# Optimization experiments

Hardware: AMD Instinct MI355X
Metric: run time of the kernel (lower is better)

The kernel has to match this reference:

```python
import jax, jax.numpy as jnp
import numpy as np

# ViT-Tiny + Performer attention (eval mode: dropout/droppath are no-ops)
B = 64
IMG, PATCH, GRID = 224, 16, 14
NPATCH, NTOK = 196, 197
EMBED, HEADS, HEAD_DIM = 192, 3, 64
DEPTH, FEAT, MLP, NCLS = 12, 256, 768, 1000
EXIT_IDXS = [4, 8, 12]
LN_EPS = 1e-5


def _ln(x, w, b):
    mu = x.mean(-1, keepdims=True)
    var = ((x - mu) ** 2).mean(-1, keepdims=True)
    return (x - mu) / jnp.sqrt(var + LN_EPS) * w + b


def setup_inputs() -> dict:
    key = jax.random.key(0)
    ks = jax.random.split(key, 16)
    n = lambda k, shape, s=0.02: jax.random.normal(k, shape, jnp.float32) * s
    inp = {}
    inp["x"] = jax.random.normal(ks[0], (B, 3, IMG, IMG), jnp.float32)
    inp["patch_w"] = n(ks[1], (EMBED, 3, PATCH, PATCH))
    inp["patch_b"] = jnp.zeros((EMBED,), jnp.float32)
    inp["pe_norm_w"] = jnp.ones((EMBED,), jnp.float32)
    inp["pe_norm_b"] = jnp.zeros((EMBED,), jnp.float32)
    inp["cls_token"] = n(ks[2], (1, 1, EMBED))
    inp["pos_embed"] = n(ks[3], (1, NTOK, EMBED))
    inp["norm1_w"] = jnp.ones((DEPTH, EMBED), jnp.float32)
    inp["norm1_b"] = jnp.zeros((DEPTH, EMBED), jnp.float32)
    inp["qkv_w"] = n(ks[4], (DEPTH, EMBED, 3 * EMBED))
    inp["qkv_b"] = jnp.zeros((DEPTH, 3 * EMBED), jnp.float32)
    # Gaussian random projection matrix (stands in for the orthogonal RF matrix)
    inp["proj_mat"] = jax.random.normal(ks[5], (DEPTH, FEAT, HEAD_DIM), jnp.float32)
    inp["attn_proj_w"] = n(ks[6], (DEPTH, EMBED, EMBED))
    inp["attn_proj_b"] = jnp.zeros((DEPTH, EMBED), jnp.float32)
    inp["norm2_w"] = jnp.ones((DEPTH, EMBED), jnp.float32)
    inp["norm2_b"] = jnp.zeros((DEPTH, EMBED), jnp.float32)
    inp["fc1_w"] = n(ks[7], (DEPTH, EMBED, MLP))
    inp["fc1_b"] = jnp.zeros((DEPTH, MLP), jnp.float32)
    inp["fc2_w"] = n(ks[8], (DEPTH, MLP, EMBED))
    inp["fc2_b"] = jnp.zeros((DEPTH, EMBED), jnp.float32)
    inp["exit_w"] = n(ks[9], (len(EXIT_IDXS), EMBED, NCLS))
    inp["exit_b"] = jnp.zeros((len(EXIT_IDXS), NCLS), jnp.float32)
    inp["final_norm_w"] = jnp.ones((EMBED,), jnp.float32)
    inp["final_norm_b"] = jnp.zeros((EMBED,), jnp.float32)
    inp["head_w"] = n(ks[10], (EMBED, NCLS))
    inp["head_b"] = jnp.zeros((NCLS,), jnp.float32)
    return inp


def _performer_attn(x, qw, qb, pm, pw, pb):
    Bn, N, C = x.shape
    qkv = (x @ qw + qb).reshape(Bn, N, 3, HEADS, HEAD_DIM).transpose(2, 0, 3, 1, 4)
    q, k, v = qkv[0], qkv[1], qkv[2]  # [B,H,N,d]

    def fmap(t):
        proj = jnp.einsum('bhnd,fd->bhnf', t, pm)  # random-feature projection
        norm_t = jnp.sum(t * t, axis=-1, keepdims=True) / 2.0
        return jnp.exp(proj - norm_t) * (HEAD_DIM ** -0.25)

    pq = fmap(q)  # [B,H,N,F]
    pk = fmap(k)
    k_cumsum = pk.sum(axis=2)  # [B,H,F]
    D_inv = 1.0 / jnp.einsum('bhnf,bhf->bhn', pq, k_cumsum)
    attn = jnp.einsum('bhnf,bhmf->bhnm', pq, pk)  # as in original (materializes NxN)
    out = jnp.einsum('bhnm,bhmd->bhnd', attn, v)
    out = out * D_inv[..., None]
    out = out.transpose(0, 2, 1, 3).reshape(Bn, N, C)
    return out @ pw + pb


def reference(x, patch_w, patch_b, pe_norm_w, pe_norm_b, cls_token, pos_embed,
              norm1_w, norm1_b, qkv_w, qkv_b, proj_mat, attn_proj_w, attn_proj_b,
              norm2_w, norm2_b, fc1_w, fc1_b, fc2_w, fc2_b,
              exit_w, exit_b, final_norm_w, final_norm_b, head_w, head_b):
    Bn = x.shape[0]
    # PatchEmbed: non-overlapping 16x16 conv == reshape + matmul (c,ph,pw order)
    p = x.reshape(Bn, 3, GRID, PATCH, GRID, PATCH).transpose(0, 2, 4, 1, 3, 5)
    p = p.reshape(Bn, NPATCH, 3 * PATCH * PATCH)
    tok = p @ patch_w.reshape(EMBED, -1).T + patch_b
    tok = _ln(tok, pe_norm_w, pe_norm_b)
    cls = jnp.broadcast_to(cls_token, (Bn, 1, EMBED))
    h = jnp.concatenate([cls, tok], axis=1) + pos_embed  # [B,197,192]

    exits = []
    for i in range(DEPTH):
        a = _performer_attn(_ln(h, norm1_w[i], norm1_b[i]), qkv_w[i], qkv_b[i],
                            proj_mat[i], attn_proj_w[i], attn_proj_b[i])
        h = h + a
        m = _ln(h, norm2_w[i], norm2_b[i])
        m = jax.nn.gelu(m @ fc1_w[i] + fc1_b[i], approximate=False) @ fc2_w[i] + fc2_b[i]
        h = h + m
        if (i + 1) in EXIT_IDXS:
            e = EXIT_IDXS.index(i + 1)
            z = h.mean(axis=1)  # AdaptiveAvgPool1d(1) over tokens
            exits.append(z @ exit_w[e] + exit_b[e])

    hf = _ln(h, final_norm_w, final_norm_b)
    logits = hf[:, 0] @ head_w + head_b  # cls-token head
    return (logits, exits[0], exits[1], exits[2])
```

## Files before the change

### kernel.cpp

```cpp
#include <hip/hip_runtime.h>
#include <math.h>

typedef unsigned short u16;
typedef unsigned int u32;
typedef __attribute__((ext_vector_type(8))) short short8;
typedef __attribute__((ext_vector_type(4))) float floatx4;

#define BB 64
#define NTOK 197
#define NPATCH 196
#define EMB 192
#define NH 3
#define HD 64
#define FEAT 256
#define MLPD 768
#define NCLS 1000
#define MTOT (BB*NTOK)
#define MPAT (BB*NPATCH)
#define BHT (BB*NH)

__device__ __forceinline__ u16 f2bf(float x) {
    u32 u = __builtin_bit_cast(u32, x);
    u32 r = u + 0x7FFFu + ((u >> 16) & 1u);
    return (u16)(r >> 16);
}
__device__ __forceinline__ float bf2f(u16 u) {
    return __builtin_bit_cast(float, (u32)u << 16);
}
__device__ __forceinline__ float sqr8bf(uint4 v) {
    float s = 0.f;
    float t;
    t = bf2f((u16)(v.x & 0xffff)); s += t*t;  t = bf2f((u16)(v.x >> 16)); s += t*t;
    t = bf2f((u16)(v.y & 0xffff)); s += t*t;  t = bf2f((u16)(v.y >> 16)); s += t*t;
    t = bf2f((u16)(v.z & 0xffff)); s += t*t;  t = bf2f((u16)(v.z >> 16)); s += t*t;
    t = bf2f((u16)(v.w & 0xffff)); s += t*t;  t = bf2f((u16)(v.w >> 16)); s += t*t;
    return s;
}

__global__ void cvt_bf16(const float* __restrict__ in, u16* __restrict__ out, int n)
{
    const int i = blockIdx.x * 256 + threadIdx.x;
    if (i < n) out[i] = f2bf(in[i]);
}

__global__ void tr_bf16(const float* __restrict__ in, u16* __restrict__ out,
                        int R, int C, int total)
{
    const int i = blockIdx.x * 256 + threadIdx.x;
    if (i >= total) return;
    const int r = i % R;
    const int c = (i / R) % C;
    const int l = i / (R * C);
    out[i] = f2bf(in[((size_t)l * R + r) * C + c]);
}

__global__ void tr_bf16_t(const float* __restrict__ in, u16* __restrict__ out,
                          int R, int C)
{
    __shared__ u16 t[32][33];
    const int l = blockIdx.z;
    const int c0 = blockIdx.x * 32, r0 = blockIdx.y * 32;
    const int tx = threadIdx.x & 31, ty = threadIdx.x >> 5;
    const float* ip = in + ((size_t)l * R + r0) * C + c0;
#pragma unroll
    for (int j = 0; j < 4; ++j)
        t[ty + j*8][tx] = f2bf(ip[(size_t)(ty + j*8) * C + tx]);
    __syncthreads();
    u16* op = out + ((size_t)l * C + c0) * R + r0;
#pragma unroll
    for (int j = 0; j < 4; ++j)
        op[(size_t)(ty + j*8) * R + tx] = t[tx][ty + j*8];
}

__global__ __launch_bounds__(256) void gemm_bf16(
    const u16* __restrict__ A, const u16* __restrict__ Bt,
    const float* __restrict__ bias,
    float* __restrict__ Cf, u16* __restrict__ Cb,
    int M, int N, int K, int mode, int ntx)
{
    __shared__ u16 As[128][72];
    __shared__ u16 Bs[64][72];
    const int tid = threadIdx.x;
    const int lane = tid & 63, wave = tid >> 6;
    const int l16 = lane & 15, quad = lane >> 4;
    const int nwg = gridDim.x;
    const int q = nwg >> 3, r = nwg & 7;
    const int xcd = blockIdx.x & 7, jj = blockIdx.x >> 3;
    const int wg = (xcd < r ? xcd * (q + 1) : r * (q + 1) + (xcd - r) * q) + jj;
    const int m0 = (wg / ntx) * 128, n0 = (wg % ntx) * 64;
    const int arow = tid >> 1, aof = (tid & 1) * 32;
    const int brow = tid >> 2, bof = (tid & 3) * 16;

    floatx4 acc[2][4];
#pragma unroll
    for (int i = 0; i < 2; ++i)
#pragma unroll
        for (int j = 0; j < 4; ++j) acc[i][j] = (floatx4){0.f,0.f,0.f,0.f};

    const int gmA = m0 + arow;
    const bool aok = (gmA < M);
    const u16* ap = A + (size_t)gmA * K + aof;
    const u16* bp = Bt + (size_t)(n0 + brow) * K + bof;

    for (int k0 = 0; k0 < K; k0 += 64) {
        uint4 a0 = {0,0,0,0}, a1 = {0,0,0,0}, a2 = {0,0,0,0}, a3 = {0,0,0,0};
        if (aok) {
            a0 = *(const uint4*)(ap + k0);
            a1 = *(const uint4*)(ap + k0 + 8);
            a2 = *(const uint4*)(ap + k0 + 16);
            a3 = *(const uint4*)(ap + k0 + 24);
        }
        const uint4 b0 = *(const uint4*)(bp + k0);
        const uint4 b1 = *(const uint4*)(bp + k0 + 8);
        if (k0) __syncthreads();
        *(uint4*)&As[arow][aof]      = a0;
        *(uint4*)&As[arow][aof + 8]  = a1;
        *(uint4*)&As[arow][aof + 16] = a2;
        *(uint4*)&As[arow][aof + 24] = a3;
        *(uint4*)&Bs[brow][bof]      = b0;
        *(uint4*)&Bs[brow][bof + 8]  = b1;
        __syncthreads();
#pragma unroll
        for (int ks = 0; ks < 2; ++ks) {
            short8 af[2], bf[4];
#pragma unroll
            for (int rf = 0; rf < 2; ++rf)
                af[rf] = *(const short8*)&As[wave*32 + rf*16 + l16][ks*32 + quad*8];
#pragma unroll
            for (int cf = 0; cf < 4; ++cf)
                bf[cf] = *(const short8*)&Bs[cf*16 + l16][ks*32 + quad*8];
#pragma unroll
            for (int rf = 0; rf < 2; ++rf)
#pragma unroll
                for (int cf = 0; cf < 4; ++cf)
                    acc[rf][cf] = __builtin_amdgcn_mfma_f32_16x16x32_bf16(af[rf], bf[cf], acc[rf][cf], 0, 0, 0);
        }
    }

    if (mode == 0) {
        const int rbase = m0 + wave * 32 + quad * 4;
        const int cbase = n0 + l16;
#pragma unroll
        for (int rf = 0; rf < 2; ++rf) {
#pragma unroll
            for (int reg = 0; reg < 4; ++reg) {
                const int gm = rbase + rf * 16 + reg;
                if (gm >= M) continue;
#pragma unroll
                for (int cf = 0; cf < 4; ++cf) {
                    const int gn = cbase + cf * 16;
                    Cf[(size_t)gm * N + gn] = acc[rf][cf][reg] + bias[gn];
                }
            }
        }
        return;
    }

    __syncthreads();
#pragma unroll
    for (int rf = 0; rf < 2; ++rf) {
#pragma unroll
        for (int cf = 0; cf < 4; ++cf) {
            const int lc = cf * 16 + l16;
            const float bia = bias[n0 + lc];
#pragma unroll
            for (int reg = 0; reg < 4; ++reg) {
                const int lr = wave * 32 + rf * 16 + quad * 4 + reg;
                float v = acc[rf][cf][reg] + bia;
                if (mode == 2)
                    v = 0.5f * v * (1.f + erff(v * 0.70710678118654752f));
                const int phys = (((lc >> 3) ^ (lr & 7)) << 3) | (lc & 7);
                As[lr][phys] = f2bf(v);
            }
        }
    }
    __syncthreads();
#pragma unroll
    for (int it = 0; it < 4; ++it) {
        const int idx = it * 256 + tid;
        const int row = idx >> 3, c8 = idx & 7;
        const int pc8 = c8 ^ (row & 7);
        const uint4 val = *(const uint4*)&As[row][pc8 * 8];
        const int gm = m0 + row;
        if (gm < M)
            *(uint4*)&Cb[(size_t)gm * N + n0 + c8 * 8] = val;
    }
}

__global__ __launch_bounds__(256) void gemm_ln(
    const u16* __restrict__ A, const u16* __restrict__ Bt,
    const float* __restrict__ bias,
    const float* __restrict__ lnw, const float* __restrict__ lnb,
    float* __restrict__ H, u16* __restrict__ outb, int K)
{
    __shared__ u16 As[32][72];
    __shared__ u16 Bs[192][72];
    __shared__ float red_s[2][32][2];
    const int tid = threadIdx.x;
    const int lane = tid & 63, wave = tid >> 6;
    const int wr = wave & 1;
    const int wc = wave >> 1;
    const int l16 = lane & 15, quad = lane >> 4;
    const int m0 = blockIdx.x * 32;
    const int srowA = tid >> 3, skofA = (tid & 7) * 8;
    const int srow = tid >> 2, skof = (tid & 3) * 16;

    floatx4 acc[6];
#pragma unroll
    for (int j = 0; j < 6; ++j) acc[j] = (floatx4){0.f,0.f,0.f,0.f};

    const u16* ap = A + (size_t)(m0 + srowA) * K + skofA;
    const u16* bp = Bt + (size_t)srow * K + skof;
    const size_t bstep = (size_t)64 * K;

    for (int k0 = 0; k0 < K; k0 += 64) {
        const uint4 a0 = *(const uint4*)(ap + k0);
        const uint4 b0 = *(const uint4*)(bp + k0);
        const uint4 b1 = *(const uint4*)(bp + k0 + 8);
        const uint4 b2 = *(const uint4*)(bp + bstep + k0);
        const uint4 b3 = *(const uint4*)(bp + bstep + k0 + 8);
        const uint4 b4 = *(const uint4*)(bp + 2*bstep + k0);
        const uint4 b5 = *(const uint4*)(bp + 2*bstep + k0 + 8);
        if (k0) __syncthreads();
        *(uint4*)&As[srowA][skofA]         = a0;
        *(uint4*)&Bs[srow][skof]           = b0;
        *(uint4*)&Bs[srow][skof + 8]       = b1;
        *(uint4*)&Bs[srow + 64][skof]      = b2;
        *(uint4*)&Bs[srow + 64][skof + 8]  = b3;
        *(uint4*)&Bs[srow + 128][skof]     = b4;
        *(uint4*)&Bs[srow + 128][skof + 8] = b5;
        __syncthreads();
#pragma unroll
        for (int ks = 0; ks < 2; ++ks) {
            const short8 af = *(const short8*)&As[wr*16 + l16][ks*32 + quad*8];
            short8 bf[6];
#pragma unroll
            for (int cf = 0; cf < 6; ++cf)
                bf[cf] = *(const short8*)&Bs[wc*96 + cf*16 + l16][ks*32 + quad*8];
#pragma unroll
            for (int cf = 0; cf < 6; ++cf)
                acc[cf] = __builtin_amdgcn_mfma_f32_16x16x32_bf16(af, bf[cf], acc[cf], 0, 0, 0);
        }
    }

    float s_[4], q_[4];
#pragma unroll
    for (int reg = 0; reg < 4; ++reg) { s_[reg] = 0.f; q_[reg] = 0.f; }

#pragma unroll
    for (int cf = 0; cf < 6; ++cf) {
        const int gn = wc * 96 + cf * 16 + l16;
        const float bia = bias[gn];
#pragma unroll
        for (int reg = 0; reg < 4; ++reg) {
            const int gm = m0 + wr * 16 + quad * 4 + reg;
            float v = acc[cf][reg] + bia + H[(size_t)gm * EMB + gn];
            H[(size_t)gm * EMB + gn] = v;
            acc[cf][reg] = v;
            s_[reg] += v;
            q_[reg] += v * v;
        }
    }

    if (lnw) {
#pragma unroll
        for (int reg = 0; reg < 4; ++reg) {
            float s = s_[reg], q = q_[reg];
            s += __shfl_xor(s, 1); q += __shfl_xor(q, 1);
            s += __shfl_xor(s, 2); q += __shfl_xor(q, 2);
            s += __shfl_xor(s, 4); q += __shfl_xor(q, 4);
            s += __shfl_xor(s, 8); q += __shfl_xor(q, 8);
            if (l16 == 0) {
                const int rl = wr * 16 + quad * 4 + reg;
                red_s[wc][rl][0] = s;
                red_s[wc][rl][1] = q;
            }
        }
        __syncthreads();
#pragma unroll
        for (int reg = 0; reg < 4; ++reg) {
            const int rl = wr * 16 + quad * 4 + reg;
            const float ts = red_s[0][rl][0] + red_s[1][rl][0];
            const float tq = red_s[0][rl][1] + red_s[1][rl][1];
            const float mu = ts * (1.f / 192.f);
            const float var = tq * (1.f / 192.f) - mu * mu;
            const float rstd = rsqrtf(fmaxf(var, 0.f) + 1e-5f);
            const int gm = m0 + rl;
#pragma unroll
            for (int cf = 0; cf < 6; ++cf) {
                const int gn = wc * 96 + cf * 16 + l16;
                const float y = (acc[cf][reg] - mu) * rstd * lnw[gn] + lnb[gn];
                outb[(size_t)gm * EMB + gn] = f2bf(y);
            }
        }
    }
}

__global__ __launch_bounds__(256) void attn_pkv(
    const u16* __restrict__ qkv, const u16* __restrict__ pmb,
    u16* __restrict__ kvT, float* __restrict__ ksum)
{
    __shared__ u16 pm_s[64][72];
    __shared__ u16 kt_s[64][72];
    __shared__ u16 vT_s[64][72];
    __shared__ u16 pkT_s[64][72];
    __shared__ float nrm_s[64];
    __shared__ float ksum_s[64];

    const int tid = threadIdx.x;
    const int lane = tid & 63, wave = tid >> 6;
    const int l16 = lane & 15, quad = lane >> 4;
    const int fq = blockIdx.x, bh = blockIdx.y, b = bh / NH, h = bh % NH;
    const int fwave = wave * 16;
    const int srow = tid >> 2, skof = (tid & 3) * 16;
    const float scale = 0.35355339059327373f;

#pragma unroll
    for (int j = 0; j < 2; ++j) {
        const int flat = j * 256 + tid;
        const int row = flat >> 3, o = (flat & 7) * 8;
        *(uint4*)&pm_s[row][o] = *(const uint4*)(pmb + (size_t)(fq * 64 + row) * 64 + o);
    }
    if (tid < 64) ksum_s[tid] = 0.f;

    floatx4 kv[4];
#pragma unroll
    for (int i = 0; i < 4; ++i) kv[i] = (floatx4){0.f,0.f,0.f,0.f};

    uint4 k0v = {0,0,0,0}, k1v = {0,0,0,0}, v0v = {0,0,0,0}, v1v = {0,0,0,0};
    {
        const u16* kp = qkv + ((size_t)(b * NTOK + srow)) * 576 + 192 + h * 64 + skof;
        k0v = *(const uint4*)kp; k1v = *(const uint4*)(kp + 8);
        v0v = *(const uint4*)(kp + 192); v1v = *(const uint4*)(kp + 200);
    }

    for (int t = 0; t < 4; ++t) {
        const int ncur = t * 64 + srow;
        if (t) __syncthreads();
        *(uint4*)&kt_s[srow][skof]     = k0v;
        *(uint4*)&kt_s[srow][skof + 8] = k1v;
        {
            u16 vv[16];
            vv[0]=(u16)(v0v.x&0xffff);  vv[1]=(u16)(v0v.x>>16);
            vv[2]=(u16)(v0v.y&0xffff);  vv[3]=(u16)(v0v.y>>16);
            vv[4]=(u16)(v0v.z&0xffff);  vv[5]=(u16)(v0v.z>>16);
            vv[6]=(u16)(v0v.w&0xffff);  vv[7]=(u16)(v0v.w>>16);
            vv[8]=(u16)(v1v.x&0xffff);  vv[9]=(u16)(v1v.x>>16);
            vv[10]=(u16)(v1v.y&0xffff); vv[11]=(u16)(v1v.y>>16);
            vv[12]=(u16)(v1v.z&0xffff); vv[13]=(u16)(v1v.z>>16);
            vv[14]=(u16)(v1v.w&0xffff); vv[15]=(u16)(v1v.w>>16);
#pragma unroll
            for (int j = 0; j < 16; ++j) vT_s[skof + j][srow] = vv[j];
        }
        float sq = sqr8bf(k0v) + sqr8bf(k1v);
        sq += __shfl_xor(sq, 1);
        sq += __shfl_xor(sq, 2);
        if ((tid & 3) == 0) nrm_s[srow] = (ncur < NTOK) ? 0.5f * sq : 1e30f;
        __syncthreads();

        if (t < 3) {
            const int n = (t + 1) * 64 + srow;
            k0v = (uint4){0,0,0,0}; k1v = (uint4){0,0,0,0};
            v0v = (uint4){0,0,0,0}; v1v = (uint4){0,0,0,0};
            if (n < NTOK) {
                const u16* kp = qkv + ((size_t)(b * NTOK + n)) * 576 + 192 + h * 64 + skof;
                k0v = *(const uint4*)kp; k1v = *(const uint4*)(kp + 8);
                v0v = *(const uint4*)(kp + 192); v1v = *(const uint4*)(kp + 200);
            }
        }

        floatx4 pa[4];
#pragma unroll
        for (int i = 0; i < 4; ++i) pa[i] = (floatx4){0.f,0.f,0.f,0.f};
#pragma unroll
        for (int ks = 0; ks < 2; ++ks) {
            const short8 bpm = *(const short8*)&pm_s[fwave + l16][ks*32 + quad*8];
#pragma unroll
            for (int rf = 0; rf < 4; ++rf) {
                const short8 a = *(const short8*)&kt_s[rf*16 + l16][ks*32 + quad*8];
                pa[rf] = __builtin_amdgcn_mfma_f32_16x16x32_bf16(a, bpm, pa[rf], 0, 0, 0);
            }
        }

        float ksp = 0.f;
        const int floc = fwave + l16;
#pragma unroll
        for (int rf = 0; rf < 4; ++rf) {
            const int nl = rf * 16 + quad * 4;
            const u16 b0 = f2bf(__expf(pa[rf][0] - nrm_s[nl + 0]) * scale);
            const u16 b1 = f2bf(__expf(pa[rf][1] - nrm_s[nl + 1]) * scale);
            const u16 b2 = f2bf(__expf(pa[rf][2] - nrm_s[nl + 2]) * scale);
            const u16 b3 = f2bf(__expf(pa[rf][3] - nrm_s[nl + 3]) * scale);
            ksp += bf2f(b0) + bf2f(b1) + bf2f(b2) + bf2f(b3);
            *(u32*)&pkT_s[floc][nl]     = (u32)b0 | ((u32)b1 << 16);
            *(u32*)&pkT_s[floc][nl + 2] = (u32)b2 | ((u32)b3 << 16);
        }
        {
            float v = ksp;
            v += __shfl_xor(v, 16);
            v += __shfl_xor(v, 32);
            if (quad == 0) ksum_s[floc] += v;
        }

#pragma unroll
        for (int ks = 0; ks < 2; ++ks) {
            const short8 bpk = *(const short8*)&pkT_s[fwave + l16][ks*32 + quad*8];
#pragma unroll
            for (int rf = 0; rf < 4; ++rf) {
                const short8 a = *(const short8*)&vT_s[rf*16 + l16][ks*32 + quad*8];
                kv[rf] = __builtin_amdgcn_mfma_f32_16x16x32_bf16(a, bpk, kv[rf], 0, 0, 0);
            }
        }
    }

    __syncthreads();
    if (tid < 64) ksum[(size_t)bh * 256 + fq * 64 + tid] = ksum_s[tid];
    const int fg = fq * 64 + fwave + l16;
#pragma unroll
    for (int rf = 0; rf < 4; ++rf) {
#pragma unroll
        for (int reg = 0; reg < 4; ++reg) {
            const int d = rf * 16 + quad * 4 + reg;
            kvT[((size_t)bh * 64 + d) * 256 + fg] = f2bf(kv[rf][reg]);
        }
    }
}

__global__ __launch_bounds__(256) void attn_out(
    const u16* __restrict__ qkv, const u16* __restrict__ pmb,
    const u16* __restrict__ kvT, const float* __restrict__ ksum,
    u16* __restrict__ attn_o)
{
    __shared__ u16 pm_s[256][72];
    __shared__ u16 q_s[64][72];
    __shared__ u16 pq_s[64][264];
    __shared__ u16 kv_s[64][264];
    __shared__ float nrm_s[64];
    __shared__ float den_s[4][64];

    const int tid = threadIdx.x;
    const int lane = tid & 63, wave = tid >> 6;
    const int l16 = lane & 15, quad = lane >> 4;
    const int bh = blockIdx.y, b = bh / NH, h = bh % NH;
    const int n0 = blockIdx.x * 64;
    const int fbase = wave * 64;
    const int srow = tid >> 2, skof = (tid & 3) * 16;
    const float scale = 0.35355339059327373f;

#pragma unroll
    for (int j = 0; j < 8; ++j) {
        const int flat = j * 256 + tid;
        const int f = flat >> 3, o = (flat & 7) * 8;
        *(uint4*)&pm_s[f][o] = *(const uint4*)(pmb + f * 64 + o);
    }
#pragma unroll
    for (int j = 0; j < 8; ++j) {
        const int flat = j * 256 + tid;
        const int d = flat >> 5, o = (flat & 31) * 8;
        *(uint4*)&kv_s[d][o] = *(const uint4*)(kvT + ((size_t)bh * 64 + d) * 256 + o);
    }
    {
        const int n = n0 + srow;
        uint4 q0 = {0,0,0,0}, q1 = {0,0,0,0};
        if (n < NTOK) {
            const u16* qp = qkv + ((size_t)(b * NTOK + n)) * 576 + h * 64 + skof;
            q0 = *(const uint4*)qp; q1 = *(const uint4*)(qp + 8);
        }
        *(uint4*)&q_s[srow][skof]     = q0;
        *(uint4*)&q_s[srow][skof + 8] = q1;
        float sq = sqr8bf(q0) + sqr8bf(q1);
        sq += __shfl_xor(sq, 1);
        sq += __shfl_xor(sq, 2);
        if ((tid & 3) == 0) nrm_s[srow] = (n < NTOK) ? 0.5f * sq : 1e30f;
    }
    float ksr[4];
#pragma unroll
    for (int cf = 0; cf < 4; ++cf)
        ksr[cf] = ksum[(size_t)bh * 256 + fbase + cf * 16 + l16];
    __syncthreads();

    floatx4 pa[4][4];
#pragma unroll
    for (int i = 0; i < 4; ++i)
#pragma unroll
        for (int j = 0; j < 4; ++j) pa[i][j] = (floatx4){0.f,0.f,0.f,0.f};
#pragma unroll
    for (int ks = 0; ks < 2; ++ks) {
        short8 a[4], bb[4];
#pragma unroll
        for (int rf = 0; rf < 4; ++rf)
            a[rf] = *(const short8*)&q_s[rf*16 + l16][ks*32 + quad*8];
#pragma unroll
        for (int cf = 0; cf < 4; ++cf)
            bb[cf] = *(const short8*)&pm_s[fbase + cf*16 + l16][ks*32 + quad*8];
#pragma unroll
        for (int rf = 0; rf < 4; ++rf)
#pragma unroll
            for (int cf = 0; cf < 4; ++cf)
                pa[rf][cf] = __builtin_amdgcn_mfma_f32_16x16x32_bf16(a[rf], bb[cf], pa[rf][cf], 0, 0, 0);
    }

    float dpart[16];
#pragma unroll
    for (int i = 0; i < 16; ++i) dpart[i] = 0.f;
#pragma unroll
    for (int rf = 0; rf < 4; ++rf) {
        const int nl = rf * 16 + quad * 4;
        const float nr0 = nrm_s[nl + 0], nr1 = nrm_s[nl + 1];
        const float nr2 = nrm_s[nl + 2], nr3 = nrm_s[nl + 3];
#pragma unroll
        for (int cf = 0; cf < 4; ++cf) {
            const int f = fbase + cf * 16 + l16;
            const u16 b0 = f2bf(__expf(pa[rf][cf][0] - nr0) * scale);
            const u16 b1 = f2bf(__expf(pa[rf][cf][1] - nr1) * scale);
            const u16 b2 = f2bf(__expf(pa[rf][cf][2] - nr2) * scale);
            const u16 b3 = f2bf(__expf(pa[rf][cf][3] - nr3) * scale);
            pq_s[nl + 0][f] = b0;
            pq_s[nl + 1][f] = b1;
            pq_s[nl + 2][f] = b2;
            pq_s[nl + 3][f] = b3;
            dpart[rf*4 + 0] += bf2f(b0) * ksr[cf];
            dpart[rf*4 + 1] += bf2f(b1) * ksr[cf];
            dpart[rf*4 + 2] += bf2f(b2) * ksr[cf];
            dpart[rf*4 + 3] += bf2f(b3) * ksr[cf];
        }
    }
#pragma unroll
    for (int i = 0; i < 16; ++i) {
        float d = dpart[i];
        d += __shfl_xor(d, 1); d += __shfl_xor(d, 2);
        d += __shfl_xor(d, 4); d += __shfl_xor(d, 8);
        dpart[i] = d;
    }
    if (l16 == 0) {
#pragma unroll
        for (int rf = 0; rf < 4; ++rf)
#pragma unroll
            for (int reg = 0; reg < 4; ++reg)
                den_s[wave][rf*16 + quad*4 + reg] = dpart[rf*4 + reg];
    }
    __syncthreads();

    const int wr = wave & 1, wc = wave >> 1;
    floatx4 oc[2][2];
#pragma unroll
    for (int i = 0; i < 2; ++i)
#pragma unroll
        for (int j = 0; j < 2; ++j) oc[i][j] = (floatx4){0.f,0.f,0.f,0.f};
#pragma unroll
    for (int ks = 0; ks < 8; ++ks) {
        short8 a[2], bb[2];
#pragma unroll
        for (int rf = 0; rf < 2; ++rf)
            a[rf] = *(const short8*)&pq_s[wr*32 + rf*16 + l16][ks*32 + quad*8];
#pragma unroll
        for (int cf = 0; cf < 2; ++cf)
            bb[cf] = *(const short8*)&kv_s[wc*32 + cf*16 + l16][ks*32 + quad*8];
#pragma unroll
        for (int rf = 0; rf < 2; ++rf)
#pragma unroll
            for (int cf = 0; cf < 2; ++cf)
                oc[rf][cf] = __builtin_amdgcn_mfma_f32_16x16x32_bf16(a[rf], bb[cf], oc[rf][cf], 0, 0, 0);
    }

#pragma unroll
    for (int rf = 0; rf < 2; ++rf) {
#pragma unroll
        for (int reg = 0; reg < 4; ++reg) {
            const int nl = wr*32 + rf*16 + quad*4 + reg;
            const int gn = n0 + nl;
            if (gn >= NTOK) continue;
            const float di = 1.f / (den_s[0][nl] + den_s[1][nl] + den_s[2][nl] + den_s[3][nl]);
#pragma unroll
            for (int cf = 0; cf < 2; ++cf) {
                const int d = wc*32 + cf*16 + l16;
                attn_o[((size_t)(b * NTOK + gn)) * EMB + h * 64 + d] =
                    f2bf(oc[rf][cf][reg] * di);
            }
        }
    }
}

__global__ void im2col_kernel(const float* __restrict__ x, u16* __restrict__ p, int total)
{
    const int i = blockIdx.x * 256 + threadIdx.x;
    if (i >= total) return;
    const int col = i % 768, row = i / 768;
    const int px = col & 15, py = (col >> 4) & 15, c = col >> 8;
    const int gx = row % 14, gy = (row / 14) % 14, b = row / 196;
    p[i] = f2bf(x[((size_t)(b * 3 + c) * 224 + gy * 16 + py) * 224 + gx * 16 + px]);
}

__global__ void embed_finish(const float* __restrict__ tok, const float* __restrict__ cls,
                             const float* __restrict__ pos, const float* __restrict__ w,
                             const float* __restrict__ b,
                             const float* __restrict__ n1w, const float* __restrict__ n1b,
                             float* __restrict__ h, u16* __restrict__ outb)
{
    const int wid = threadIdx.x >> 6, lane = threadIdx.x & 63;
    const int r = blockIdx.x * 4 + wid;
    if (r >= MTOT) return;
    const int bb = r / NTOK, t = r % NTOK;
    float y0, y1, y2;
    if (t == 0) {
        y0 = cls[lane]       + pos[lane];
        y1 = cls[lane + 64]  + pos[lane + 64];
        y2 = cls[lane + 128] + pos[lane + 128];
    } else {
        const float* p = tok + ((size_t)bb * NPATCH + (t - 1)) * EMB;
        float x0 = p[lane], x1 = p[lane + 64], x2 = p[lane + 128];
        float s = x0 + x1 + x2;
#pragma unroll
        for (int off = 32; off; off >>= 1) s += __shfl_xor(s, off);
        const float mu = s * (1.f / 192.f);
        const float d0 = x0 - mu, d1 = x1 - mu, d2 = x2 - mu;
        float v = d0 * d0 + d1 * d1 + d2 * d2;
#pragma unroll
        for (int off = 32; off; off >>= 1) v += __shfl_xor(v, off);
        const float rstd = rsqrtf(v * (1.f / 192.f) + 1e-5f);
        const float* pr = pos + (size_t)t * EMB;
        y0 = d0 * rstd * w[lane]       + b[lane]       + pr[lane];
        y1 = d1 * rstd * w[lane + 64]  + b[lane + 64]  + pr[lane + 64];
        y2 = d2 * rstd * w[lane + 128] + b[lane + 128] + pr[lane + 128];
    }
    float* q = h + (size_t)r * EMB;
    q[lane] = y0; q[lane + 64] = y1; q[lane + 128] = y2;
    float s2 = y0 + y1 + y2;
#pragma unroll
    for (int off = 32; off; off >>= 1) s2 += __shfl_xor(s2, off);
    const float mu2 = s2 * (1.f / 192.f);
    const float e0 = y0 - mu2, e1 = y1 - mu2, e2 = y2 - mu2;
    float v2 = e0 * e0 + e1 * e1 + e2 * e2;
#pragma unroll
    for (int off = 32; off; off >>= 1) v2 += __shfl_xor(v2, off);
    const float rstd2 = rsqrtf(v2 * (1.f / 192.f) + 1e-5f);
    u16* o = outb + (size_t)r * EMB;
    o[lane]       = f2bf(e0 * rstd2 * n1w[lane]       + n1b[lane]);
    o[lane + 64]  = f2bf(e1 * rstd2 * n1w[lane + 64]  + n1b[lane + 64]);
    o[lane + 128] = f2bf(e2 * rstd2 * n1w[lane + 128] + n1b[lane + 128]);
}

__global__ void ln192(const float* __restrict__ in, int in_stride,
                      const float* __restrict__ w, const float* __restrict__ b,
                      u16* __restrict__ outb, float* __restrict__ outf, int rows)
{
    const int wid = threadIdx.x >> 6, lane = threadIdx.x & 63;
    const int r = blockIdx.x * 4 + wid;
    if (r >= rows) return;
    const float* p = in + (size_t)r * in_stride;
    float x0 = p[lane], x1 = p[lane + 64], x2 = p[lane + 128];
    float s = x0 + x1 + x2;
#pragma unroll
    for (int off = 32; off; off >>= 1) s += __shfl_xor(s, off);
    const float mu = s * (1.f / 192.f);
    const float d0 = x0 - mu, d1 = x1 - mu, d2 = x2 - mu;
    float v = d0 * d0 + d1 * d1 + d2 * d2;
#pragma unroll
    for (int off = 32; off; off >>= 1) v += __shfl_xor(v, off);
    const float rstd = rsqrtf(v * (1.f / 192.f) + 1e-5f);
    const float y0 = d0 * rstd * w[lane]       + b[lane];
    const float y1 = d1 * rstd * w[lane + 64]  + b[lane + 64];
    const float y2 = d2 * rstd * w[lane + 128] + b[lane + 128];
    if (outf) {
        float* q = outf + (size_t)r * EMB;
        q[lane] = y0; q[lane + 64] = y1; q[lane + 128] = y2;
    } else {
        u16* q = outb + (size_t)r * EMB;
        q[lane] = f2bf(y0); q[lane + 64] = f2bf(y1); q[lane + 128] = f2bf(y2);
    }
}

__global__ __launch_bounds__(256) void gemm_cls(
    const u16* __restrict__ A, const u16* __restrict__ Bt,
    const float* __restrict__ bias, float* __restrict__ C,
    int N, int K)
{
    __shared__ u16 As[64][72];
    __shared__ u16 Bs[64][72];
    const int tid = threadIdx.x;
    const int lane = tid & 63, wave = tid >> 6;
    const int wr = wave & 1, wc = wave >> 1;
    const int l16 = lane & 15, quad = lane >> 4;
    const int n0 = blockIdx.x * 64;
    const int srow = tid >> 2, skof = (tid & 3) * 16;

    floatx4 acc[2][2];
#pragma unroll
    for (int i = 0; i < 2; ++i)
#pragma unroll
        for (int j = 0; j < 2; ++j) acc[i][j] = (floatx4){0.f,0.f,0.f,0.f};

    const u16* ap = A + (size_t)srow * K + skof;
    int brow_g = n0 + srow;  if (brow_g > N - 1) brow_g = N - 1;
    const u16* bp = Bt + (size_t)brow_g * K + skof;

    for (int k0 = 0; k0 < K; k0 += 64) {
        const uint4 a0 = *(const uint4*)(ap + k0);
        const uint4 a1 = *(const uint4*)(ap + k0 + 8);
        const uint4 b0 = *(const uint4*)(bp + k0);
        const uint4 b1 = *(const uint4*)(bp + k0 + 8);
        if (k0) __syncthreads();
        *(uint4*)&As[srow][skof]     = a0;
        *(uint4*)&As[srow][skof + 8] = a1;
        *(uint4*)&Bs[srow][skof]     = b0;
        *(uint4*)&Bs[srow][skof + 8] = b1;
        __syncthreads();
#pragma unroll
        for (int ks = 0; ks < 2; ++ks) {
            short8 af[2], bf[2];
#pragma unroll
            for (int rf = 0; rf < 2; ++rf)
                af[rf] = *(const short8*)&As[wr*32 + rf*16 + l16][ks*32 + quad*8];
#pragma unroll
            for (int cf = 0; cf < 2; ++cf)
                bf[cf] = *(const short8*)&Bs[wc*32 + cf*16 + l16][ks*32 + quad*8];
#pragma unroll
            for (int rf = 0; rf < 2; ++rf)
#pragma unroll
                for (int cf = 0; cf < 2; ++cf)
                    acc[rf][cf] = __builtin_amdgcn_mfma_f32_16x16x32_bf16(af[rf], bf[cf], acc[rf][cf], 0, 0, 0);
        }
    }

#pragma unroll
    for (int rf = 0; rf < 2; ++rf) {
#pragma unroll
        for (int reg = 0; reg < 4; ++reg) {
            const int gm = wr*32 + rf*16 + quad*4 + reg;
#pragma unroll
            for (int cf = 0; cf < 2; ++cf) {
                const int gn = n0 + wc*32 + cf*16 + l16;
                if (gn < N)
                    C[(size_t)gm * N + gn] = acc[rf][cf][reg] + bias[gn];
            }
        }
    }
}

__global__ void pool_kernel(const float* __restrict__ h, u16* __restrict__ pooled)
{
    __shared__ float red[192];
    const int b = blockIdx.x;
    const int slice = threadIdx.x / 192;
    const int e = threadIdx.x % 192;
    float s = 0.f;
    for (int n = slice; n < NTOK; n += 2)
        s += h[((size_t)(b * NTOK + n)) * EMB + e];
    if (slice == 1) red[e] = s;
    __syncthreads();
    if (slice == 0)
        pooled[b * EMB + e] = f2bf((s + red[e]) * (1.f / 197.f));
}

extern "C" void kernel_launch(void* const* d_in, const int* in_sizes, int n_in,
                              void* d_out, int out_size, void* d_ws, size_t ws_size,
                              hipStream_t stream)
{
    const float* x          = (const float*)d_in[0];
    const float* patch_w    = (const float*)d_in[1];
    const float* patch_b    = (const float*)d_in[2];
    const float* pe_norm_w  = (const float*)d_in[3];
    const float* pe_norm_b  = (const float*)d_in[4];
    const float* cls_token  = (const float*)d_in[5];
    const float* pos_embed  = (const float*)d_in[6];
    const float* norm1_w    = (const float*)d_in[7];
    const float* norm1_b    = (const float*)d_in[8];
    const float* qkv_w      = (const float*)d_in[9];
    const float* qkv_b      = (const float*)d_in[10];
    const float* proj_mat   = (const float*)d_in[11];
    const float* attn_pw    = (const float*)d_in[12];
    const float* attn_pb    = (const float*)d_in[13];
    const float* norm2_w    = (const float*)d_in[14];
    const float* norm2_b    = (const float*)d_in[15];
    const float* fc1_w      = (const float*)d_in[16];
    const float* fc1_b      = (const float*)d_in[17];
    const float* fc2_w      = (const float*)d_in[18];
    const float* fc2_b      = (const float*)d_in[19];
    const float* exit_w     = (const float*)d_in[20];
    const float* exit_b     = (const float*)d_in[21];
    const float* fnorm_w    = (const float*)d_in[22];
    const float* fnorm_b    = (const float*)d_in[23];
    const float* head_w     = (const float*)d_in[24];
    const float* head_b     = (const float*)d_in[25];
    float* out = (float*)d_out;

    float* ws = (float*)d_ws;
    float* H     = ws + 0;
    u16*   QKVB  = (u16*)(ws + 2420736);
    u16*   XLNB  = (u16*)(ws + 6051840);
    u16*   EXWT  = (u16*)(ws + 7262208);
    u16*   HWT   = (u16*)(ws + 7550208);
    u16*   POOLB = (u16*)(ws + 7646208);
    u16*   KVT   = (u16*)(ws + 19968000);
    u16*   MIDB  = (u16*)(ws + 21540864);
    u16*   ATNB  = (u16*)(ws + 26382336);
    float* KSUM  = ws + 27617280;
    u16*   QKVWT = (u16*)(ws + 27666432);
    u16*   APWT  = (u16*)(ws + 28329984);
    u16*   F1WT  = (u16*)(ws + 28551168);
    u16*   F2WT  = (u16*)(ws + 29435904);
    u16*   PATWB = (u16*)(ws + 30320640);
    u16*   PMB   = (u16*)(ws + 30394368);
    u16*   P_IMB = MIDB;
    float* TOK   = (float*)QKVB;

    if (ws_size < (size_t)30492672 * sizeof(float)) return;

    cvt_bf16<<<(147456 + 255) / 256, 256, 0, stream>>>(patch_w, PATWB, 147456);
    cvt_bf16<<<(196608 + 255) / 256, 256, 0, stream>>>(proj_mat, PMB, 196608);
    tr_bf16_t<<<dim3(18, 6, 12), 256, 0, stream>>>(qkv_w,   QKVWT, 192, 576);
    tr_bf16_t<<<dim3(6, 6, 12),  256, 0, stream>>>(attn_pw, APWT,  192, 192);
    tr_bf16_t<<<dim3(24, 6, 12), 256, 0, stream>>>(fc1_w,   F1WT,  192, 768);
    tr_bf16_t<<<dim3(6, 24, 12), 256, 0, stream>>>(fc2_w,   F2WT,  768, 192);
    tr_bf16<<<(576000 + 255) / 256, 256, 0, stream>>>(exit_w, EXWT, 192, 1000, 576000);
    tr_bf16<<<(192000 + 255) / 256, 256, 0, stream>>>(head_w, HWT,  192, 1000, 192000);

    im2col_kernel<<<(MPAT * 768 + 255) / 256, 256, 0, stream>>>(x, P_IMB, MPAT * 768);
    gemm_bf16<<<294, 256, 0, stream>>>(P_IMB, PATWB, patch_b,
                                       TOK, nullptr, MPAT, EMB, 768, 0, 3);
    embed_finish<<<(MTOT + 3) / 4, 256, 0, stream>>>(TOK, cls_token, pos_embed,
                                                     pe_norm_w, pe_norm_b,
                                                     norm1_w, norm1_b, H, XLNB);

    for (int i = 0; i < 12; ++i) {
        const u16* qwt  = QKVWT + (size_t)i * 576 * 192;
        const u16* pwt  = APWT  + (size_t)i * 192 * 192;
        const u16* f1wt = F1WT  + (size_t)i * 768 * 192;
        const u16* f2wt = F2WT  + (size_t)i * 192 * 768;
        const u16* pmb  = PMB   + (size_t)i * 256 * 64;
        const float* qb  = qkv_b   + (size_t)i * 576;
        const float* pb  = attn_pb + (size_t)i * 192;
        const float* f1b = fc1_b   + (size_t)i * 768;

        gemm_bf16<<<891, 256, 0, stream>>>(XLNB, qwt, qb,
                                           nullptr, QKVB, MTOT, 576, 192, 3, 9);
        attn_pkv<<<dim3(4, BHT), 256, 0, stream>>>(QKVB, pmb, KVT, KSUM);
        attn_out<<<dim3(4, BHT), 256, 0, stream>>>(QKVB, pmb, KVT, KSUM, ATNB);
        gemm_ln<<<394, 256, 0, stream>>>(ATNB, pwt, pb,
                                         norm2_w + (size_t)i * EMB, norm2_b + (size_t)i * EMB,
                                         H, XLNB, EMB);
        gemm_bf16<<<1188, 256, 0, stream>>>(XLNB, f1wt, f1b,
                                            nullptr, MIDB, MTOT, MLPD, 192, 2, 12);
        const float* nw = (i < 11) ? norm1_w + (size_t)(i + 1) * EMB : nullptr;
        const float* nb = (i < 11) ? norm1_b + (size_t)(i + 1) * EMB : nullptr;
        gemm_ln<<<394, 256, 0, stream>>>(MIDB, f2wt, fc2_b + (size_t)i * 192,
                                         nw, nb, H, XLNB, MLPD);

        const int e = (i == 3) ? 0 : (i == 7) ? 1 : (i == 11) ? 2 : -1;
        if (e >= 0) {
            pool_kernel<<<BB, 384, 0, stream>>>(H, POOLB);
            gemm_cls<<<16, 256, 0, stream>>>(POOLB, EXWT + (size_t)e * 1000 * 192,
                                             exit_b + (size_t)e * 1000,
                                             out + (size_t)(1 + e) * BB * NCLS,
                                             NCLS, EMB);
        }
    }

    ln192<<<(BB + 3) / 4, 256, 0, stream>>>(H, NTOK * EMB, fnorm_w, fnorm_b,
                                            XLNB, nullptr, BB);
    gemm_cls<<<16, 256, 0, stream>>>(XLNB, HWT, head_b, out, NCLS, EMB);
}
```

Baseline: 1.391 ms.

## Fuse fc1, GELU, fc2, residual and LayerNorm into one MLP kernel

Adds an mlp_ln kernel in which each block keeps 32 token rows resident. It streams 64-wide chunks of the fc1 and fc2 weights through LDS, applies GELU in registers, and accumulates fc2 before doing the residual add and the next LayerNorm. This removes the bf16 round trip of the 768-wide hidden activation through global memory and drops one launch per layer. The cost is that every block re-reads all weights from cache, and the kernel now has many synchronisations, no double buffering and low occupancy with about 70KB of LDS per block. The exit and head weight transposes also move to a tiled shared-memory transpose kernel, a small one-time setup change.

```diff
diff --git a/kernel.cpp b/kernel.cpp
--- a/kernel.cpp
+++ b/kernel.cpp
@@ -43,17 +43,6 @@
     if (i < n) out[i] = f2bf(in[i]);
 }
 
-__global__ void tr_bf16(const float* __restrict__ in, u16* __restrict__ out,
-                        int R, int C, int total)
-{
-    const int i = blockIdx.x * 256 + threadIdx.x;
-    if (i >= total) return;
-    const int r = i % R;
-    const int c = (i / R) % C;
-    const int l = i / (R * C);
-    out[i] = f2bf(in[((size_t)l * R + r) * C + c]);
-}
-
 __global__ void tr_bf16_t(const float* __restrict__ in, u16* __restrict__ out,
                           int R, int C)
 {
@@ -70,6 +59,29 @@
 #pragma unroll
     for (int j = 0; j < 4; ++j)
         op[(size_t)(ty + j*8) * R + tx] = t[tx][ty + j*8];
+}
+
+__global__ void tr_bf16_g(const float* __restrict__ in, u16* __restrict__ out,
+                          int R, int C)
+{
+    __shared__ u16 t[32][33];
+    const int l = blockIdx.z;
+    const int c0 = blockIdx.x * 32, r0 = blockIdx.y * 32;
+    const int tx = threadIdx.x & 31, ty = threadIdx.x >> 5;
+    const float* ip = in + (size_t)l * R * C;
+#pragma unroll
+    for (int j = 0; j < 4; ++j) {
+        const int r = r0 + ty + j*8, c = c0 + tx;
+        t[ty + j*8][tx] = (r < R && c < C) ? f2bf(ip[(size_t)r * C + c]) : (u16)0;
+    }
+    __syncthreads();
+    u16* op = out + (size_t)l * C * R;
+#pragma unroll
+    for (int j = 0; j < 4; ++j) {
+        const int c = c0 + ty + j*8, r = r0 + tx;
+        if (c < C && r < R)
+            op[(size_t)c * R + r] = t[tx][ty + j*8];
+    }
 }
 
 __global__ __launch_bounds__(256) void gemm_bf16(
@@ -166,9 +178,7 @@
 #pragma unroll
             for (int reg = 0; reg < 4; ++reg) {
                 const int lr = wave * 32 + rf * 16 + quad * 4 + reg;
-                float v = acc[rf][cf][reg] + bia;
-                if (mode == 2)
-                    v = 0.5f * v * (1.f + erff(v * 0.70710678118654752f));
+                const float v = acc[rf][cf][reg] + bia;
                 const int phys = (((lc >> 3) ^ (lr & 7)) << 3) | (lc & 7);
                 As[lr][phys] = f2bf(v);
             }
@@ -291,6 +301,161 @@
                 const int gn = wc * 96 + cf * 16 + l16;
                 const float y = (acc[cf][reg] - mu) * rstd * lnw[gn] + lnb[gn];
                 outb[(size_t)gm * EMB + gn] = f2bf(y);
+            }
+        }
+    }
+}
+
+__global__ __launch_bounds__(256) void mlp_ln(
+    const u16* __restrict__ A, const u16* __restrict__ W1t,
+    const float* __restrict__ b1,
+    const u16* __restrict__ W2t, const float* __restrict__ b2,
+    const float* __restrict__ lnw, const float* __restrict__ lnb,
+    float* __restrict__ H, u16* __restrict__ outb)
+{
+    __shared__ u16 As[32][200];
+    __shared__ u16 W1s[64][200];
+    __shared__ u16 W2s[192][72];
+    __shared__ u16 Ms[32][72];
+    __shared__ float red_s[4][32][2];
+    const int tid = threadIdx.x;
+    const int lane = tid & 63, wave = tid >> 6;
+    const int l16 = lane & 15, quad = lane >> 4;
+    const int m0 = blockIdx.x * 32;
+
+    {
+        const int row = tid >> 3, cb = (tid & 7) * 24;
+        const u16* ap = A + (size_t)(m0 + row) * EMB + cb;
+#pragma unroll
+        for (int j = 0; j < 3; ++j)
+            *(uint4*)&As[row][cb + j * 8] = *(const uint4*)(ap + j * 8);
+    }
+    __syncthreads();
+    short8 af[2][6];
+#pragma unroll
+    for (int rf = 0; rf < 2; ++rf)
+#pragma unroll
+        for (int ks = 0; ks < 6; ++ks)
+            af[rf][ks] = *(const short8*)&As[rf*16 + l16][ks*32 + quad*8];
+
+    floatx4 acc[2][3];
+#pragma unroll
+    for (int i = 0; i < 2; ++i)
+#pragma unroll
+        for (int j = 0; j < 3; ++j) acc[i][j] = (floatx4){0.f,0.f,0.f,0.f};
+
+    for (int c = 0; c < 12; ++c) {
+        if (c) __syncthreads();
+        {
+            const int row = tid >> 2, cb = (tid & 3) * 48;
+            const u16* wp = W1t + (size_t)(c * 64 + row) * EMB + cb;
+#pragma unroll
+            for (int j = 0; j < 6; ++j)
+                *(uint4*)&W1s[row][cb + j * 8] = *(const uint4*)(wp + j * 8);
+        }
+#pragma unroll
+        for (int j = 0; j < 6; ++j) {
+            const int idx = j * 256 + tid;
+            const int e = idx >> 3, o = (idx & 7) * 8;
+            *(uint4*)&W2s[e][o] = *(const uint4*)(W2t + (size_t)e * MLPD + c * 64 + o);
+        }
+        __syncthreads();
+
+        floatx4 mf[2] = {(floatx4){0.f,0.f,0.f,0.f}, (floatx4){0.f,0.f,0.f,0.f}};
+#pragma unroll
+        for (int ks = 0; ks < 6; ++ks) {
+            const short8 w1f = *(const short8*)&W1s[wave*16 + l16][ks*32 + quad*8];
+            mf[0] = __builtin_amdgcn_mfma_f32_16x16x32_bf16(af[0][ks], w1f, mf[0], 0, 0, 0);
+            mf[1] = __builtin_amdgcn_mfma_f32_16x16x32_bf16(af[1][ks], w1f, mf[1], 0, 0, 0);
+        }
+        const float bia = b1[c * 64 + wave * 16 + l16];
+#pragma unroll
+        for (int rf = 0; rf < 2; ++rf)
+#pragma unroll
+            for (int reg = 0; reg < 4; ++reg) {
+                float v = mf[rf][reg] + bia;
+                v = 0.5f * v * (1.f + erff(v * 0.70710678118654752f));
+                Ms[rf*16 + quad*4 + reg][wave*16 + l16] = f2bf(v);
+            }
+        __syncthreads();
+
+#pragma unroll
+        for (int ks2 = 0; ks2 < 2; ++ks2) {
+            short8 a2[2], w2f[3];
+#pragma unroll
+            for (int rf = 0; rf < 2; ++rf)
+                a2[rf] = *(const short8*)&Ms[rf*16 + l16][ks2*32 + quad*8];
+#pragma unroll
+            for (int cf = 0; cf < 3; ++cf)
+                w2f[cf] = *(const short8*)&W2s[wave*48 + cf*16 + l16][ks2*32 + quad*8];
+#pragma unroll
+            for (int rf = 0; rf < 2; ++rf)
+#pragma unroll
+                for (int cf = 0; cf < 3; ++cf)
+                    acc[rf][cf] = __builtin_amdgcn_mfma_f32_16x16x32_bf16(a2[rf], w2f[cf], acc[rf][cf], 0, 0, 0);
+        }
+    }
+
+    float s_[2][4], q_[2][4];
+#pragma unroll
+    for (int rf = 0; rf < 2; ++rf)
+#pragma unroll
+        for (int reg = 0; reg < 4; ++reg) { s_[rf][reg] = 0.f; q_[rf][reg] = 0.f; }
+
+#pragma unroll
+    for (int rf = 0; rf < 2; ++rf) {
+#pragma unroll
+        for (int cf = 0; cf < 3; ++cf) {
+            const int gn = wave * 48 + cf * 16 + l16;
+            const float bia = b2[gn];
+#pragma unroll
+            for (int reg = 0; reg < 4; ++reg) {
+                const int gm = m0 + rf * 16 + quad * 4 + reg;
+                float v = acc[rf][cf][reg] + bia + H[(size_t)gm * EMB + gn];
+                H[(size_t)gm * EMB + gn] = v;
+                acc[rf][cf][reg] = v;
+                s_[rf][reg] += v;
+                q_[rf][reg] += v * v;
+            }
+        }
+    }
+
+    if (lnw) {
+#pragma unroll
+        for (int rf = 0; rf < 2; ++rf)
+#pragma unroll
+            for (int reg = 0; reg < 4; ++reg) {
+                float s = s_[rf][reg], q = q_[rf][reg];
+                s += __shfl_xor(s, 1); q += __shfl_xor(q, 1);
+                s += __shfl_xor(s, 2); q += __shfl_xor(q, 2);
+                s += __shfl_xor(s, 4); q += __shfl_xor(q, 4);
+                s += __shfl_xor(s, 8); q += __shfl_xor(q, 8);
+                if (l16 == 0) {
+                    const int rl = rf * 16 + quad * 4 + reg;
+                    red_s[wave][rl][0] = s;
+                    red_s[wave][rl][1] = q;
+                }
+            }
+        __syncthreads();
+#pragma unroll
+        for (int rf = 0; rf < 2; ++rf) {
+#pragma unroll
+            for (int reg = 0; reg < 4; ++reg) {
+                const int rl = rf * 16 + quad * 4 + reg;
+                const float ts = red_s[0][rl][0] + red_s[1][rl][0]
+                               + red_s[2][rl][0] + red_s[3][rl][0];
+                const float tq = red_s[0][rl][1] + red_s[1][rl][1]
+                               + red_s[2][rl][1] + red_s[3][rl][1];
+                const float mu = ts * (1.f / 192.f);
+                const float var = tq * (1.f / 192.f) - mu * mu;
+                const float rstd = rsqrtf(fmaxf(var, 0.f) + 1e-5f);
+                const int gm = m0 + rl;
+#pragma unroll
+                for (int cf = 0; cf < 3; ++cf) {
+                    const int gn = wave * 48 + cf * 16 + l16;
+                    const float y = (acc[rf][cf][reg] - mu) * rstd * lnw[gn] + lnb[gn];
+                    outb[(size_t)gm * EMB + gn] = f2bf(y);
+                }
             }
         }
     }
@@ -812,8 +977,8 @@
     tr_bf16_t<<<dim3(6, 6, 12),  256, 0, stream>>>(attn_pw, APWT,  192, 192);
     tr_bf16_t<<<dim3(24, 6, 12), 256, 0, stream>>>(fc1_w,   F1WT,  192, 768);
     tr_bf16_t<<<dim3(6, 24, 12), 256, 0, stream>>>(fc2_w,   F2WT,  768, 192);
-    tr_bf16<<<(576000 + 255) / 256, 256, 0, stream>>>(exit_w, EXWT, 192, 1000, 576000);
-    tr_bf16<<<(192000 + 255) / 256, 256, 0, stream>>>(head_w, HWT,  192, 1000, 192000);
+    tr_bf16_g<<<dim3(32, 6, 3), 256, 0, stream>>>(exit_w, EXWT, 192, 1000);
+    tr_bf16_g<<<dim3(32, 6, 1), 256, 0, stream>>>(head_w, HWT,  192, 1000);
 
     im2col_kernel<<<(MPAT * 768 + 255) / 256, 256, 0, stream>>>(x, P_IMB, MPAT * 768);
     gemm_bf16<<<294, 256, 0, stream>>>(P_IMB, PATWB, patch_b,
@@ -839,12 +1004,10 @@
         gemm_ln<<<394, 256, 0, stream>>>(ATNB, pwt, pb,
                                          norm2_w + (size_t)i * EMB, norm2_b + (size_t)i * EMB,
                                          H, XLNB, EMB);
-        gemm_bf16<<<1188, 256, 0, stream>>>(XLNB, f1wt, f1b,
-                                            nullptr, MIDB, MTOT, MLPD, 192, 2, 12);
         const float* nw = (i < 11) ? norm1_w + (size_t)(i + 1) * EMB : nullptr;
         const float* nb = (i < 11) ? norm1_b + (size_t)(i + 1) * EMB : nullptr;
-        gemm_ln<<<394, 256, 0, stream>>>(MIDB, f2wt, fc2_b + (size_t)i * 192,
-                                         nw, nb, H, XLNB, MLPD);
+        mlp_ln<<<394, 256, 0, stream>>>(XLNB, f1wt, f1b, f2wt,
+                                        fc2_b + (size_t)i * 192, nw, nb, H, XLNB);
 
         const int e = (i == 3) ? 0 : (i == 7) ? 1 : (i == 11) ? 2 : -1;
         if (e >= 0) {
```

New measurement: 1.350 ms. -2.9%, faster.
